# Performance work log

Hardware: AMD Instinct MI355X
Metric: run time of the kernel (lower is better)

Reference implementation:

```python
import jax, jax.numpy as jnp
import numpy as np


def setup_inputs() -> dict:
    key = jax.random.key(0)
    kq, kk, kv = jax.random.split(key, 3)
    G, B, H, S, D = 4, 2, 16, 1024, 64  # ring size, batch, heads, seq_local, dim_head
    shape = (G, B, H, S, D)
    q = jax.random.normal(kq, shape, dtype=jnp.float32)
    k = jax.random.normal(kk, shape, dtype=jnp.float32)
    v = jax.random.normal(kv, shape, dtype=jnp.float32)
    return {"q": q, "k": k, "v": v}


def reference(q, k, v):
    """Ring attention with online (logsumexp) softmax merge.

    q, k, v: [G, B, H, S_local, D] where G is the number of ring participants.
    Each ring step: every participant attends its local Q against the currently
    visiting K/V chunk, then K/V chunks rotate around the ring (roll on axis 0).
    """
    G = q.shape[0]
    scale = 1.0 / np.sqrt(q.shape[-1]).astype(np.float32)
    out = jnp.zeros_like(q)
    # running logsumexp per query: [G, B, H, S, 1]
    lse = jnp.full(q.shape[:-1] + (1,), -jnp.inf, dtype=q.dtype)
    cur_k, cur_v = k, v
    for ring_step in range(G):
        # [G,B,H,Sq,Sk] chunk attention scores
        scores = jnp.einsum('gbhqd,gbhkd->gbhqk', q, cur_k) * scale
        chunk_max = scores.max(axis=-1, keepdims=True)
        chunk_exp = jnp.exp(scores - chunk_max)
        chunk_sum = chunk_exp.sum(axis=-1, keepdims=True)
        chunk_lse = chunk_max + jnp.log(chunk_sum)
        chunk_out = jnp.einsum('gbhqk,gbhkd->gbhqd', chunk_exp / chunk_sum, cur_v)
        # online merge via logaddexp rescaling
        new_lse = jnp.logaddexp(lse, chunk_lse)
        out = out * jnp.exp(lse - new_lse) + chunk_out * jnp.exp(chunk_lse - new_lse)
        lse = new_lse
        if ring_step < G - 1:
            # next_k[i] = current_k[i-1]  ->  roll +1 along ring axis
            cur_k = jnp.roll(cur_k, 1, axis=0)
            cur_v = jnp.roll(cur_v, 1, axis=0)
    return out
```

## Files before the change

kernel.cpp:

```cpp
#include <hip/hip_runtime.h>
#include <stdint.h>


#define RG 4
#define RB 2
#define RH 16
#define RS 1024
#define RD 64

using bf16x8 = __attribute__((ext_vector_type(8))) short;
using bf16x4 = __attribute__((ext_vector_type(4))) short;
using f16x8  = __attribute__((ext_vector_type(8))) _Float16;
using f16x2  = __attribute__((ext_vector_type(2))) _Float16;
using f32x4  = __attribute__((ext_vector_type(4))) float;
using u32x2  = __attribute__((ext_vector_type(2))) uint32_t;
using u32x4  = __attribute__((ext_vector_type(4))) uint32_t;

#if __has_builtin(__builtin_amdgcn_mfma_f32_16x16x16_bf16)
#define MFMA_PV(a, b, c) __builtin_amdgcn_mfma_f32_16x16x16_bf16(a, b, c, 0, 0, 0)
#else
#define MFMA_PV(a, b, c) __builtin_amdgcn_mfma_f32_16x16x16bf16_1k(a, b, c, 0, 0, 0)
#endif

#if __has_builtin(__builtin_amdgcn_exp2f)
#define EXP2F(x) __builtin_amdgcn_exp2f(x)
#else
#define EXP2F(x) exp2f(x)
#endif

__device__ inline uint16_t f2bf(float x) {
    uint32_t u = __float_as_uint(x);
    u += 0x7fffu + ((u >> 16) & 1u);
    return (uint16_t)(u >> 16);
}
__device__ inline float bf2f(uint16_t b) {
    return __uint_as_float(((uint32_t)b) << 16);
}
__device__ inline uint32_t pkbf2(float lo, float hi) {
    uint32_t a = __float_as_uint(lo) + 0x8000u;
    uint32_t b = __float_as_uint(hi) + 0x8000u;
    return (a >> 16) | (b & 0xffff0000u);
}
__device__ inline uint32_t pkh2(float lo, float hi) {
#if __has_builtin(__builtin_amdgcn_cvt_pkrtz)
    return __builtin_bit_cast(uint32_t, __builtin_amdgcn_cvt_pkrtz(lo, hi));
#else
    union { _Float16 h[2]; uint32_t u; } r;
    r.h[0] = (_Float16)lo; r.h[1] = (_Float16)hi;
    return r.u;
#endif
}
__device__ inline uint4 pack8(const uint16_t* h) {
    uint4 r;
    r.x = (uint32_t)h[0] | ((uint32_t)h[1] << 16);
    r.y = (uint32_t)h[2] | ((uint32_t)h[3] << 16);
    r.z = (uint32_t)h[4] | ((uint32_t)h[5] << 16);
    r.w = (uint32_t)h[6] | ((uint32_t)h[7] << 16);
    return r;
}

__global__ __launch_bounds__(256)
void prep_kv(const float* __restrict__ k, const float* __restrict__ v,
             uint16_t* __restrict__ kf, uint16_t* __restrict__ vf) {
    __shared__ uint16_t kl[64 * 72];
    __shared__ uint16_t vl[64 * 72];
    const int bid = blockIdx.x;
    const int hc = bid >> 4, kt = bid & 15;
    const size_t base = (size_t)hc * (RS * RD) + (size_t)kt * 64 * RD;
    const int t = threadIdx.x;
    const int row = t >> 2;
    const int seg = (t & 3) * 16;

    {
        const float* src = k + base + (size_t)row * RD + seg;
        float4 a0 = ((const float4*)src)[0];
        float4 a1 = ((const float4*)src)[1];
        float4 a2 = ((const float4*)src)[2];
        float4 a3 = ((const float4*)src)[3];
        uint4 w0, w1;
        w0.x = pkh2(a0.x, a0.y); w0.y = pkh2(a0.z, a0.w);
        w0.z = pkh2(a1.x, a1.y); w0.w = pkh2(a1.z, a1.w);
        w1.x = pkh2(a2.x, a2.y); w1.y = pkh2(a2.z, a2.w);
        w1.z = pkh2(a3.x, a3.y); w1.w = pkh2(a3.z, a3.w);
        uint16_t* d0 = &kl[row * 72 + seg];
        ((uint4*)d0)[0] = w0; ((uint4*)d0)[1] = w1;
    }
    {
        const float* src = v + base + (size_t)row * RD + seg;
        float4 a0 = ((const float4*)src)[0];
        float4 a1 = ((const float4*)src)[1];
        float4 a2 = ((const float4*)src)[2];
        float4 a3 = ((const float4*)src)[3];
        uint4 w0, w1;
        w0.x = pkh2(a0.x, a0.y); w0.y = pkh2(a0.z, a0.w);
        w0.z = pkh2(a1.x, a1.y); w0.w = pkh2(a1.z, a1.w);
        w1.x = pkh2(a2.x, a2.y); w1.y = pkh2(a2.z, a2.w);
        w1.z = pkh2(a3.x, a3.y); w1.w = pkh2(a3.z, a3.w);
        uint16_t* d0 = &vl[row * 72 + seg];
        ((uint4*)d0)[0] = w0; ((uint4*)d0)[1] = w1;
    }
    __syncthreads();

    {
        uint4 o[2];
#pragma unroll
        for (int si = 0; si < 2; ++si) {
            const int s  = 2 * t + si;
            const int ks = s >> 8, nt = (s >> 6) & 3, ln = s & 63;
            const int key = nt * 16 + (ln & 15);
            const int d   = ks * 32 + (ln >> 4) * 8;
            o[si] = *(const uint4*)&kl[key * 72 + d];
        }
        uint16_t* dst = kf + (size_t)bid * 4096 + t * 16;
        ((uint4*)dst)[0] = o[0]; ((uint4*)dst)[1] = o[1];
    }
    {
        uint16_t ob[16];
#pragma unroll
        for (int si = 0; si < 2; ++si) {
            const int s  = 2 * t + si;
            const int dt = s >> 7, b = (s >> 6) & 1, ln = s & 63;
            const int c = ln & 15, qd = ln >> 4;
            const int d = dt * 16 + c;
#pragma unroll
            for (int j = 0; j < 8; ++j) {
                const int key = b * 32 + ((j >> 2) << 4) + qd * 4 + (j & 3);
                ob[si * 8 + j] = vl[key * 72 + d];
            }
        }
        uint16_t* dst = vf + (size_t)bid * 4096 + t * 16;
        ((uint4*)dst)[0] = pack8(ob); ((uint4*)dst)[1] = pack8(ob + 8);
    }
}

constexpr int TILE_SH = 4096;
constexpr int BUF_SH  = 2 * TILE_SH;
constexpr int SMEM4   = 2 * BUF_SH;

__global__ __launch_bounds__(256, 4)
void ring_attn_mfma5(const float* __restrict__ q, const uint16_t* __restrict__ kf_g,
                     const uint16_t* __restrict__ vf_g, float* __restrict__ out) {
    __shared__ __attribute__((aligned(16))) uint16_t smem[SMEM4];

    const int tid  = threadIdx.x;
    const int wave = tid >> 6;
    const int lane = tid & 63;
    const int quad = lane >> 4;
    const int col  = lane & 15;

    {
        uint32_t* sw = (uint32_t*)smem;
#pragma unroll
        for (int i = 0; i < SMEM4 / 2 / 256; ++i) sw[i * 256 + tid] = 0u;
    }
    __syncthreads();

    const int bid   = blockIdx.x;
    const int head  = bid & 127;
    const int qtile = bid >> 7;
    const int bh    = head & 31;

    const size_t hcq = (size_t)head * (RS * RD);
    const int qbase  = qtile * 128 + wave * 32;

    const float sc = 0.125f * 1.44269504088896340736f;

    {
        const size_t tb = (size_t)(bh * 16) * TILE_SH;
        const uint4* ks4 = (const uint4*)(kf_g + tb);
        const uint4* vs4 = (const uint4*)(vf_g + tb);
        uint4 a = ks4[tid], b = ks4[tid + 256];
        uint4 c = vs4[tid], d = vs4[tid + 256];
        uint4* dk = (uint4*)&smem[0];
        uint4* dv = (uint4*)&smem[TILE_SH];
        dk[tid] = a; dk[tid + 256] = b;
        dv[tid] = c; dv[tid + 256] = d;
    }

    f16x8 qf[2][2];
#pragma unroll
    for (int mt = 0; mt < 2; ++mt)
#pragma unroll
        for (int ks = 0; ks < 2; ++ks) {
            const float* qp = q + hcq + (size_t)(qbase + mt * 16 + col) * RD + ks * 32 + quad * 8;
            float4 t0 = ((const float4*)qp)[0];
            float4 t1 = ((const float4*)qp)[1];
            u32x4 w = {pkh2(t0.x * sc, t0.y * sc), pkh2(t0.z * sc, t0.w * sc),
                       pkh2(t1.x * sc, t1.y * sc), pkh2(t1.z * sc, t1.w * sc)};
            qf[mt][ks] = __builtin_bit_cast(f16x8, w);
        }

    f32x4 oacc[2][4];
#pragma unroll
    for (int mt = 0; mt < 2; ++mt)
#pragma unroll
        for (int dt = 0; dt < 4; ++dt) oacc[mt][dt] = (f32x4){0.f, 0.f, 0.f, 0.f};
    float lrun[2] = {0.f, 0.f};

    __syncthreads();

    int cur = 0;
    for (int it = 0; it < (RG * RS) / 64; ++it) {
        const bool pre = (it < (RG * RS) / 64 - 1);
        const uint4* ks4 = nullptr;
        const uint4* vs4 = nullptr;
        uint4 stk0, stk1, stv0, stv1;
        if (pre) {
            const int nit = it + 1;
            const size_t tb =
                (size_t)((((nit >> 4) * 32 + bh) << 4) + (nit & 15)) * TILE_SH;
            ks4 = (const uint4*)(kf_g + tb);
            vs4 = (const uint4*)(vf_g + tb);
            stk0 = ks4[tid]; stk1 = ks4[tid + 256];
        }

        const uint16_t* kbuf = &smem[cur * BUF_SH];
        const uint16_t* vbuf = kbuf + TILE_SH;

        f32x4 sacc[2][4];
#pragma unroll
        for (int mt = 0; mt < 2; ++mt)
#pragma unroll
            for (int nt = 0; nt < 4; ++nt) sacc[mt][nt] = (f32x4){0.f, 0.f, 0.f, 0.f};
        __builtin_amdgcn_s_setprio(1);
#pragma unroll
        for (int nt = 0; nt < 4; ++nt) {
            f16x8 kfr[2];
            kfr[0] = *(const f16x8*)&kbuf[(size_t)((0 * 4 + nt) * 64 + lane) * 8];
            kfr[1] = *(const f16x8*)&kbuf[(size_t)((1 * 4 + nt) * 64 + lane) * 8];
#pragma unroll
            for (int mt = 0; mt < 2; ++mt)
#pragma unroll
                for (int ks = 0; ks < 2; ++ks)
                    sacc[mt][nt] = __builtin_amdgcn_mfma_f32_16x16x32_f16(kfr[ks], qf[mt][ks], sacc[mt][nt], 0, 0, 0);
        }
        __builtin_amdgcn_s_setprio(0);

        if (pre) {
            uint4* dk = (uint4*)&smem[(cur ^ 1) * BUF_SH];
            dk[tid] = stk0; dk[tid + 256] = stk1;
            stv0 = vs4[tid]; stv1 = vs4[tid + 256];
        }

        f16x8 pf[2][2];
#pragma unroll
        for (int mt = 0; mt < 2; ++mt) {
            float ls = 0.f;
            uint32_t w[4][2];
#pragma unroll
            for (int nt = 0; nt < 4; ++nt) {
                float p0 = EXP2F(sacc[mt][nt][0]);
                float p1 = EXP2F(sacc[mt][nt][1]);
                float p2 = EXP2F(sacc[mt][nt][2]);
                float p3 = EXP2F(sacc[mt][nt][3]);
                ls += (p0 + p1) + (p2 + p3);
                w[nt][0] = pkh2(p0, p1);
                w[nt][1] = pkh2(p2, p3);
            }
            u32x4 b0 = {w[0][0], w[0][1], w[1][0], w[1][1]};
            u32x4 b1 = {w[2][0], w[2][1], w[3][0], w[3][1]};
            pf[mt][0] = __builtin_bit_cast(f16x8, b0);
            pf[mt][1] = __builtin_bit_cast(f16x8, b1);
            lrun[mt] += ls;
        }

        __builtin_amdgcn_s_setprio(1);
#pragma unroll
        for (int dt = 0; dt < 4; ++dt)
#pragma unroll
            for (int b = 0; b < 2; ++b) {
                f16x8 vfr = *(const f16x8*)&vbuf[(size_t)((dt * 2 + b) * 64 + lane) * 8];
#pragma unroll
                for (int mt = 0; mt < 2; ++mt)
                    oacc[mt][dt] = __builtin_amdgcn_mfma_f32_16x16x32_f16(vfr, pf[mt][b], oacc[mt][dt], 0, 0, 0);
            }
        __builtin_amdgcn_s_setprio(0);

        if (pre) {
            uint4* dv = (uint4*)&smem[(cur ^ 1) * BUF_SH + TILE_SH];
            dv[tid] = stv0; dv[tid + 256] = stv1;
        }

        __syncthreads();
        cur ^= 1;
    }

#pragma unroll
    for (int mt = 0; mt < 2; ++mt) {
        lrun[mt] += __shfl_xor(lrun[mt], 16);
        lrun[mt] += __shfl_xor(lrun[mt], 32);
        const float inv = 1.0f / lrun[mt];
        const int qrow = qbase + mt * 16 + col;
#pragma unroll
        for (int dt = 0; dt < 4; ++dt) {
            float4 st;
            st.x = oacc[mt][dt][0] * inv;
            st.y = oacc[mt][dt][1] * inv;
            st.z = oacc[mt][dt][2] * inv;
            st.w = oacc[mt][dt][3] * inv;
            *(float4*)&out[hcq + (size_t)qrow * RD + dt * 16 + quad * 4] = st;
        }
    }
}

__global__ __launch_bounds__(256)
void prep_vt(const float* __restrict__ v, uint16_t* __restrict__ vt) {
    __shared__ uint16_t tl[64 * 72];
    const int bid = blockIdx.x;
    const int hc = bid >> 4, kt = bid & 15;
    const size_t base = (size_t)hc * (RS * RD);
    const int t = threadIdx.x;
    const int row = t >> 2;
    const int seg = (t & 3) * 16;

    const float* src = v + base + (size_t)(kt * 64 + row) * RD + seg;
    uint16_t hb[16];
#pragma unroll
    for (int i = 0; i < 4; ++i) {
        float4 x = ((const float4*)src)[i];
        hb[4 * i + 0] = f2bf(x.x); hb[4 * i + 1] = f2bf(x.y);
        hb[4 * i + 2] = f2bf(x.z); hb[4 * i + 3] = f2bf(x.w);
    }
    uint16_t* d = &tl[row * 72 + seg];
    ((uint4*)d)[0] = pack8(hb); ((uint4*)d)[1] = pack8(hb + 8);
    __syncthreads();

    uint16_t ob[16];
#pragma unroll
    for (int i = 0; i < 16; ++i) ob[i] = tl[(seg + i) * 72 + row];
    uint16_t* dst = vt + base + (size_t)row * RS + kt * 64 + seg;
    ((uint4*)dst)[0] = pack8(ob); ((uint4*)dst)[1] = pack8(ob + 8);
}

constexpr int KSTR   = 72;
constexpr int OFF_K  = 0;
constexpr int OFF_VT = 64 * KSTR;
constexpr int SMEM2  = 2 * 64 * KSTR;

__global__ __launch_bounds__(256, 4)
void ring_attn_mfma3(const float* __restrict__ q, const float* __restrict__ k_g,
                     const uint16_t* __restrict__ vt_g, float* __restrict__ out) {
    __shared__ __attribute__((aligned(16))) uint16_t smem[SMEM2];

    const int tid  = threadIdx.x;
    const int wave = tid >> 6;
    const int lane = tid & 63;
    const int quad = lane >> 4;
    const int col  = lane & 15;

    {
        uint32_t* sw = (uint32_t*)smem;
#pragma unroll
        for (int i = 0; i < SMEM2 / 2 / 256; ++i) sw[i * 256 + tid] = 0u;
    }

    const int bid   = blockIdx.x;
    const int head  = bid & 127;
    const int qtile = bid >> 7;
    const int bh    = head & 31;

    const size_t hcq = (size_t)head * (RS * RD);
    const int qbase  = qtile * 128 + wave * 32;

    const float sc = 0.125f * 1.44269504088896340736f;

    bf16x8 qh[2][2], ql[2][2];
#pragma unroll
    for (int mt = 0; mt < 2; ++mt)
#pragma unroll
        for (int ks = 0; ks < 2; ++ks) {
            const float* qp = q + hcq + (size_t)(qbase + mt * 16 + col) * RD + ks * 32 + quad * 8;
            float4 t0 = ((const float4*)qp)[0];
            float4 t1 = ((const float4*)qp)[1];
            float xs[8] = {t0.x, t0.y, t0.z, t0.w, t1.x, t1.y, t1.z, t1.w};
            bf16x8 hv, lv;
#pragma unroll
            for (int j = 0; j < 8; ++j) {
                float x = xs[j] * sc;
                uint16_t hb = f2bf(x);
                hv[j] = (short)hb;
                lv[j] = (short)f2bf(x - bf2f(hb));
            }
            qh[mt][ks] = hv;
            ql[mt][ks] = lv;
        }

    f32x4 oacc[2][4];
#pragma unroll
    for (int mt = 0; mt < 2; ++mt)
#pragma unroll
        for (int dt = 0; dt < 4; ++dt) oacc[mt][dt] = (f32x4){0.f, 0.f, 0.f, 0.f};
    float lrun[2] = {0.f, 0.f};

    const int srow = tid >> 2;
    const int sseg = (tid & 3) * 16;

    for (int it = 0; it < (RG * RS) / 64; ++it) {
        const int gp = it >> 4, ktile = it & 15;
        const size_t cbase = (size_t)(gp * 32 + bh) * (RS * RD);

        __syncthreads();
        {
            const float* kp = k_g + cbase + (size_t)(ktile * 64 + srow) * RD + sseg;
            float4 a0 = ((const float4*)kp)[0];
            float4 a1 = ((const float4*)kp)[1];
            float4 a2 = ((const float4*)kp)[2];
            float4 a3 = ((const float4*)kp)[3];
            uint4 w0, w1;
            w0.x = pkbf2(a0.x, a0.y); w0.y = pkbf2(a0.z, a0.w);
            w0.z = pkbf2(a1.x, a1.y); w0.w = pkbf2(a1.z, a1.w);
            w1.x = pkbf2(a2.x, a2.y); w1.y = pkbf2(a2.z, a2.w);
            w1.z = pkbf2(a3.x, a3.y); w1.w = pkbf2(a3.z, a3.w);
            uint16_t* d0 = &smem[OFF_K + srow * KSTR + sseg];
            ((uint4*)d0)[0] = w0;
            ((uint4*)d0)[1] = w1;
            const uint16_t* s2 = vt_g + cbase + (size_t)srow * RS + ktile * 64 + sseg;
            uint16_t* d2 = &smem[OFF_VT + srow * KSTR + sseg];
            ((uint4*)d2)[0] = ((const uint4*)s2)[0];
            ((uint4*)d2)[1] = ((const uint4*)s2)[1];
        }
        __syncthreads();

        f32x4 sacc[2][4];
#pragma unroll
        for (int mt = 0; mt < 2; ++mt)
#pragma unroll
            for (int nt = 0; nt < 4; ++nt) sacc[mt][nt] = (f32x4){0.f, 0.f, 0.f, 0.f};
#pragma unroll
        for (int nt = 0; nt < 4; ++nt) {
            bf16x8 kf[2];
#pragma unroll
            for (int ks = 0; ks < 2; ++ks)
                kf[ks] = *(const bf16x8*)&smem[OFF_K + (nt * 16 + col) * KSTR + ks * 32 + quad * 8];
#pragma unroll
            for (int mt = 0; mt < 2; ++mt)
#pragma unroll
                for (int ks = 0; ks < 2; ++ks) {
                    sacc[mt][nt] = __builtin_amdgcn_mfma_f32_16x16x32_bf16(kf[ks], qh[mt][ks], sacc[mt][nt], 0, 0, 0);
                    sacc[mt][nt] = __builtin_amdgcn_mfma_f32_16x16x32_bf16(kf[ks], ql[mt][ks], sacc[mt][nt], 0, 0, 0);
                }
        }

        bf16x4 pf[2][4];
#pragma unroll
        for (int mt = 0; mt < 2; ++mt) {
            float ls = 0.f;
#pragma unroll
            for (int nt = 0; nt < 4; ++nt) {
                float p0 = EXP2F(sacc[mt][nt][0]);
                float p1 = EXP2F(sacc[mt][nt][1]);
                float p2 = EXP2F(sacc[mt][nt][2]);
                float p3 = EXP2F(sacc[mt][nt][3]);
                ls += (p0 + p1) + (p2 + p3);
                u32x2 t;
                t[0] = pkbf2(p0, p1);
                t[1] = pkbf2(p2, p3);
                pf[mt][nt] = __builtin_bit_cast(bf16x4, t);
            }
            lrun[mt] += ls;
        }

#pragma unroll
        for (int dt = 0; dt < 4; ++dt) {
            bf16x4 vf[4];
#pragma unroll
            for (int nt = 0; nt < 4; ++nt)
                vf[nt] = *(const bf16x4*)&smem[OFF_VT + (dt * 16 + col) * KSTR + nt * 16 + quad * 4];
#pragma unroll
            for (int mt = 0; mt < 2; ++mt)
#pragma unroll
                for (int nt = 0; nt < 4; ++nt)
                    oacc[mt][dt] = MFMA_PV(vf[nt], pf[mt][nt], oacc[mt][dt]);
        }
    }

#pragma unroll
    for (int mt = 0; mt < 2; ++mt) {
        lrun[mt] += __shfl_xor(lrun[mt], 16);
        lrun[mt] += __shfl_xor(lrun[mt], 32);
        const float inv = 1.0f / lrun[mt];
        const int qrow = qbase + mt * 16 + col;
#pragma unroll
        for (int dt = 0; dt < 4; ++dt) {
            float4 st;
            st.x = oacc[mt][dt][0] * inv;
            st.y = oacc[mt][dt][1] * inv;
            st.z = oacc[mt][dt][2] * inv;
            st.w = oacc[mt][dt][3] * inv;
            *(float4*)&out[hcq + (size_t)qrow * RD + dt * 16 + quad * 4] = st;
        }
    }
}

extern "C" void kernel_launch(void* const* d_in, const int* in_sizes, int n_in,
                              void* d_out, int out_size, void* d_ws, size_t ws_size,
                              hipStream_t stream) {
    const float* q = (const float*)d_in[0];
    const float* k = (const float*)d_in[1];
    const float* v = (const float*)d_in[2];
    float* out = (float*)d_out;

    const size_t NEL = (size_t)RG * RB * RH * RS * RD;
    const size_t need2 = 2 * NEL * sizeof(uint16_t);
    const size_t need1 = NEL * sizeof(uint16_t);

    if (ws_size >= need2) {
        uint16_t* kf = (uint16_t*)d_ws;
        uint16_t* vf = kf + NEL;
        prep_kv<<<2048, 256, 0, stream>>>(k, v, kf, vf);
        ring_attn_mfma5<<<1024, 256, 0, stream>>>(q, kf, vf, out);
    } else if (ws_size >= need1) {
        uint16_t* vt = (uint16_t*)d_ws;
        prep_vt<<<2048, 256, 0, stream>>>(v, vt);
        ring_attn_mfma3<<<1024, 256, 0, stream>>>(q, k, vt, out);
    } else {
        uint16_t* vt = (uint16_t*)d_ws;
        prep_vt<<<2048, 256, 0, stream>>>(v, vt);
        ring_attn_mfma3<<<1024, 256, 0, stream>>>(q, k, vt, out);
    }
}
```

Before: 260.8 us.

## Stage K/V tiles with direct global-to-LDS loads and drop LDS from prep

The attention kernel now prefetches the next K/V tile with global_load_lds (buffer-to-LDS DMA) issued at the top of each iteration, instead of loading into registers and writing to LDS after each MFMA phase. This is meant to cut register pressure and VALU/LDS-store work, and to overlap the copy with compute. The prep kernel also drops its LDS transpose and gathers straight from global memory, which removes a barrier but uses less coalesced reads, especially the strided float2 loads for V. Correctness depends on the async LDS writes completing before the end-of-iteration barrier and on the per-wave LDS base matching the lane layout.

Measured after the change: 259.8 us. No clear change (-0.4%).

```diff
diff --git a/kernel.cpp b/kernel.cpp
--- a/kernel.cpp
+++ b/kernel.cpp
@@ -11,7 +11,6 @@
 using bf16x8 = __attribute__((ext_vector_type(8))) short;
 using bf16x4 = __attribute__((ext_vector_type(4))) short;
 using f16x8  = __attribute__((ext_vector_type(8))) _Float16;
-using f16x2  = __attribute__((ext_vector_type(2))) _Float16;
 using f32x4  = __attribute__((ext_vector_type(4))) float;
 using u32x2  = __attribute__((ext_vector_type(2))) uint32_t;
 using u32x4  = __attribute__((ext_vector_type(4))) uint32_t;
@@ -59,47 +58,22 @@
     return r;
 }
 
+__device__ inline void glds16(const uint16_t* g, uint16_t* lbase, int lane) {
+#if __has_builtin(__builtin_amdgcn_global_load_lds)
+    __builtin_amdgcn_global_load_lds(
+        (const __attribute__((address_space(1))) uint32_t*)g,
+        (__attribute__((address_space(3))) uint32_t*)lbase, 16, 0, 0);
+#else
+    *(uint4*)(lbase + lane * 8) = *(const uint4*)g;
+#endif
+}
+
 __global__ __launch_bounds__(256)
 void prep_kv(const float* __restrict__ k, const float* __restrict__ v,
              uint16_t* __restrict__ kf, uint16_t* __restrict__ vf) {
-    __shared__ uint16_t kl[64 * 72];
-    __shared__ uint16_t vl[64 * 72];
     const int bid = blockIdx.x;
-    const int hc = bid >> 4, kt = bid & 15;
-    const size_t base = (size_t)hc * (RS * RD) + (size_t)kt * 64 * RD;
     const int t = threadIdx.x;
-    const int row = t >> 2;
-    const int seg = (t & 3) * 16;
-
-    {
-        const float* src = k + base + (size_t)row * RD + seg;
-        float4 a0 = ((const float4*)src)[0];
-        float4 a1 = ((const float4*)src)[1];
-        float4 a2 = ((const float4*)src)[2];
-        float4 a3 = ((const float4*)src)[3];
-        uint4 w0, w1;
-        w0.x = pkh2(a0.x, a0.y); w0.y = pkh2(a0.z, a0.w);
-        w0.z = pkh2(a1.x, a1.y); w0.w = pkh2(a1.z, a1.w);
-        w1.x = pkh2(a2.x, a2.y); w1.y = pkh2(a2.z, a2.w);
-        w1.z = pkh2(a3.x, a3.y); w1.w = pkh2(a3.z, a3.w);
-        uint16_t* d0 = &kl[row * 72 + seg];
-        ((uint4*)d0)[0] = w0; ((uint4*)d0)[1] = w1;
-    }
-    {
-        const float* src = v + base + (size_t)row * RD + seg;
-        float4 a0 = ((const float4*)src)[0];
-        float4 a1 = ((const float4*)src)[1];
-        float4 a2 = ((const float4*)src)[2];
-        float4 a3 = ((const float4*)src)[3];
-        uint4 w0, w1;
-        w0.x = pkh2(a0.x, a0.y); w0.y = pkh2(a0.z, a0.w);
-        w0.z = pkh2(a1.x, a1.y); w0.w = pkh2(a1.z, a1.w);
-        w1.x = pkh2(a2.x, a2.y); w1.y = pkh2(a2.z, a2.w);
-        w1.z = pkh2(a3.x, a3.y); w1.w = pkh2(a3.z, a3.w);
-        uint16_t* d0 = &vl[row * 72 + seg];
-        ((uint4*)d0)[0] = w0; ((uint4*)d0)[1] = w1;
-    }
-    __syncthreads();
+    const size_t base = (size_t)bid * (64 * RD);
 
     {
         uint4 o[2];
@@ -109,27 +83,34 @@
             const int ks = s >> 8, nt = (s >> 6) & 3, ln = s & 63;
             const int key = nt * 16 + (ln & 15);
             const int d   = ks * 32 + (ln >> 4) * 8;
-            o[si] = *(const uint4*)&kl[key * 72 + d];
+            const float* sp = k + base + (size_t)key * RD + d;
+            float4 a0 = ((const float4*)sp)[0];
+            float4 a1 = ((const float4*)sp)[1];
+            o[si].x = pkh2(a0.x, a0.y); o[si].y = pkh2(a0.z, a0.w);
+            o[si].z = pkh2(a1.x, a1.y); o[si].w = pkh2(a1.z, a1.w);
         }
         uint16_t* dst = kf + (size_t)bid * 4096 + t * 16;
         ((uint4*)dst)[0] = o[0]; ((uint4*)dst)[1] = o[1];
     }
     {
-        uint16_t ob[16];
-#pragma unroll
-        for (int si = 0; si < 2; ++si) {
-            const int s  = 2 * t + si;
-            const int dt = s >> 7, b = (s >> 6) & 1, ln = s & 63;
-            const int c = ln & 15, qd = ln >> 4;
-            const int d = dt * 16 + c;
-#pragma unroll
-            for (int j = 0; j < 8; ++j) {
-                const int key = b * 32 + ((j >> 2) << 4) + qd * 4 + (j & 3);
-                ob[si * 8 + j] = vl[key * 72 + d];
-            }
-        }
+        const int s0 = 2 * t;
+        const int dt = s0 >> 7, b = (s0 >> 6) & 1, ln = s0 & 63;
+        const int c = ln & 15, qd = ln >> 4;
+        const int d = dt * 16 + c;
+        float x0[8], x1[8];
+#pragma unroll
+        for (int j = 0; j < 8; ++j) {
+            const int key = b * 32 + ((j >> 2) << 4) + qd * 4 + (j & 3);
+            float2 xv = *(const float2*)(v + base + (size_t)key * RD + d);
+            x0[j] = xv.x; x1[j] = xv.y;
+        }
+        uint4 o0, o1;
+        o0.x = pkh2(x0[0], x0[1]); o0.y = pkh2(x0[2], x0[3]);
+        o0.z = pkh2(x0[4], x0[5]); o0.w = pkh2(x0[6], x0[7]);
+        o1.x = pkh2(x1[0], x1[1]); o1.y = pkh2(x1[2], x1[3]);
+        o1.z = pkh2(x1[4], x1[5]); o1.w = pkh2(x1[6], x1[7]);
         uint16_t* dst = vf + (size_t)bid * 4096 + t * 16;
-        ((uint4*)dst)[0] = pack8(ob); ((uint4*)dst)[1] = pack8(ob + 8);
+        ((uint4*)dst)[0] = o0; ((uint4*)dst)[1] = o1;
     }
 }
 
@@ -137,8 +118,21 @@
 constexpr int BUF_SH  = 2 * TILE_SH;
 constexpr int SMEM4   = 2 * BUF_SH;
 
+__device__ inline void stage_tile(uint16_t* smem, const uint16_t* kf_g,
+                                  const uint16_t* vf_g, size_t tb,
+                                  int dbuf, int tid, int wave, int lane) {
+    const uint16_t* gk = kf_g + tb;
+    const uint16_t* gv = vf_g + tb;
+    uint16_t* lk = smem + dbuf * BUF_SH + wave * 512;
+    uint16_t* lv = smem + dbuf * BUF_SH + TILE_SH + wave * 512;
+    glds16(gk + (size_t)tid * 8,         lk,        lane);
+    glds16(gk + (size_t)(256 + tid) * 8, lk + 2048, lane);
+    glds16(gv + (size_t)tid * 8,         lv,        lane);
+    glds16(gv + (size_t)(256 + tid) * 8, lv + 2048, lane);
+}
+
 __global__ __launch_bounds__(256, 4)
-void ring_attn_mfma5(const float* __restrict__ q, const uint16_t* __restrict__ kf_g,
+void ring_attn_mfma6(const float* __restrict__ q, const uint16_t* __restrict__ kf_g,
                      const uint16_t* __restrict__ vf_g, float* __restrict__ out) {
     __shared__ __attribute__((aligned(16))) uint16_t smem[SMEM4];
 
@@ -165,17 +159,7 @@
 
     const float sc = 0.125f * 1.44269504088896340736f;
 
-    {
-        const size_t tb = (size_t)(bh * 16) * TILE_SH;
-        const uint4* ks4 = (const uint4*)(kf_g + tb);
-        const uint4* vs4 = (const uint4*)(vf_g + tb);
-        uint4 a = ks4[tid], b = ks4[tid + 256];
-        uint4 c = vs4[tid], d = vs4[tid + 256];
-        uint4* dk = (uint4*)&smem[0];
-        uint4* dv = (uint4*)&smem[TILE_SH];
-        dk[tid] = a; dk[tid + 256] = b;
-        dv[tid] = c; dv[tid + 256] = d;
-    }
+    stage_tile(smem, kf_g, vf_g, (size_t)(bh * 16) * TILE_SH, 0, tid, wave, lane);
 
     f16x8 qf[2][2];
 #pragma unroll
@@ -202,16 +186,11 @@
     int cur = 0;
     for (int it = 0; it < (RG * RS) / 64; ++it) {
         const bool pre = (it < (RG * RS) / 64 - 1);
-        const uint4* ks4 = nullptr;
-        const uint4* vs4 = nullptr;
-        uint4 stk0, stk1, stv0, stv1;
         if (pre) {
             const int nit = it + 1;
             const size_t tb =
                 (size_t)((((nit >> 4) * 32 + bh) << 4) + (nit & 15)) * TILE_SH;
-            ks4 = (const uint4*)(kf_g + tb);
-            vs4 = (const uint4*)(vf_g + tb);
-            stk0 = ks4[tid]; stk1 = ks4[tid + 256];
+            stage_tile(smem, kf_g, vf_g, tb, cur ^ 1, tid, wave, lane);
         }
 
         const uint16_t* kbuf = &smem[cur * BUF_SH];
@@ -235,12 +214,6 @@
                     sacc[mt][nt] = __builtin_amdgcn_mfma_f32_16x16x32_f16(kfr[ks], qf[mt][ks], sacc[mt][nt], 0, 0, 0);
         }
         __builtin_amdgcn_s_setprio(0);
-
-        if (pre) {
-            uint4* dk = (uint4*)&smem[(cur ^ 1) * BUF_SH];
-            dk[tid] = stk0; dk[tid + 256] = stk1;
-            stv0 = vs4[tid]; stv1 = vs4[tid + 256];
-        }
 
         f16x8 pf[2][2];
 #pragma unroll
@@ -275,11 +248,6 @@
                     oacc[mt][dt] = __builtin_amdgcn_mfma_f32_16x16x32_f16(vfr, pf[mt][b], oacc[mt][dt], 0, 0, 0);
             }
         __builtin_amdgcn_s_setprio(0);
-
-        if (pre) {
-            uint4* dv = (uint4*)&smem[(cur ^ 1) * BUF_SH + TILE_SH];
-            dv[tid] = stv0; dv[tid + 256] = stv1;
-        }
 
         __syncthreads();
         cur ^= 1;
@@ -508,7 +476,7 @@
         uint16_t* kf = (uint16_t*)d_ws;
         uint16_t* vf = kf + NEL;
         prep_kv<<<2048, 256, 0, stream>>>(k, v, kf, vf);
-        ring_attn_mfma5<<<1024, 256, 0, stream>>>(q, kf, vf, out);
+        ring_attn_mfma6<<<1024, 256, 0, stream>>>(q, kf, vf, out);
     } else if (ws_size >= need1) {
         uint16_t* vt = (uint16_t*)d_ws;
         prep_vt<<<2048, 256, 0, stream>>>(v, vt);
```
